# Kernel tuning notes

Hardware: AMD Instinct MI355X
Metric: run time of the kernel (lower is better)

Reference implementation:

```python
import jax, jax.numpy as jnp
import numpy as np
import math

B, TU, TM, D, H = 4, 2048, 256, 1024, 16
DH = D // H
PAIRS = D // 2
LAM = 0.7
EPS_PHASE = 1e-8


def balance_norm(x, w, b, bal_w):
    mu = x.mean(-1, keepdims=True)
    var = ((x - mu) ** 2).mean(-1, keepdims=True)
    normed = (x - mu) / jnp.sqrt(var + 1e-6) * w + b
    half = x.shape[-1] // 2
    e1 = (x[..., :half] ** 2).mean(-1, keepdims=True)
    e2 = (x[..., half:] ** 2).mean(-1, keepdims=True)
    imb = (e1 - e2) * bal_w  # (B,T,1)
    corr = jnp.concatenate([
        jnp.broadcast_to(-imb, x[..., :half].shape),
        jnp.broadcast_to(imb, x[..., half:].shape)], axis=-1)
    return normed + corr


def phase_resonance(a, b):
    # a: (B,Tq,D), b: (B,Tk,D). mean_p cos(th_a - th_b) == (cosA@cosB^T + sinA@sinB^T)/pairs
    def to_phase(x):
        x2 = x.reshape(*x.shape[:-1], PAIRS, 2)
        return jnp.arctan2(x2[..., 1] + EPS_PHASE, x2[..., 0] + EPS_PHASE)
    ta, tb = to_phase(a), to_phase(b)
    ca, sa = jnp.cos(ta), jnp.sin(ta)
    cb, sb = jnp.cos(tb), jnp.sin(tb)
    r = (jnp.einsum('bqp,bkp->bqk', ca, cb) + jnp.einsum('bqp,bkp->bqk', sa, sb)) / PAIRS
    return r


def mha(q_in, kv_in, wq, wk, wv, wo, a_gate, e_gate):
    Bq, Tq, _ = q_in.shape
    Tk = kv_in.shape[1]
    q = (q_in @ wq.T).reshape(Bq, Tq, H, DH)
    k = (kv_in @ wk.T).reshape(Bq, Tk, H, DH)
    v = (kv_in @ wv.T).reshape(Bq, Tk, H, DH)
    scores = jnp.einsum('bqhd,bkhd->bhqk', q, k) / math.sqrt(DH)
    attn = jax.nn.softmax(scores, axis=-1)
    ag = a_gate[:, None, :, :]              # (B,1,Tq,1)
    eg = jnp.swapaxes(e_gate[:, None], 2, 3)  # (B,1,1,Tk)
    attn = attn * ag * eg
    attn = attn / (attn.sum(-1, keepdims=True) + 1e-8)
    ctx = jnp.einsum('bhqk,bkhd->bqhd', attn, v).reshape(Bq, Tq, D)
    return ctx @ wo.T


def setup_inputs() -> dict:
    key = jax.random.key(0)
    ks = jax.random.split(key, 16)
    s = 0.02
    return {
        'o_micro': jax.random.normal(ks[0], (B, TU, D), jnp.float32),
        'o_macro': jax.random.normal(ks[1], (B, TM, D), jnp.float32),
        'r_conv_acc': jax.random.normal(ks[2], (B, TM, TU), jnp.float32) * 0.1,
        'r_emer_acc': jax.random.normal(ks[3], (B, TU, TM), jnp.float32) * 0.1,
        'ln_u_w': jnp.ones((D,), jnp.float32),
        'ln_u_b': jnp.zeros((D,), jnp.float32),
        'bw_u': jnp.float32(0.01),
        'ln_m_w': jnp.ones((D,), jnp.float32),
        'ln_m_b': jnp.zeros((D,), jnp.float32),
        'bw_m': jnp.float32(0.01),
        'gu_w': jax.random.normal(ks[4], (1, D), jnp.float32) * s,
        'gu_b': jnp.zeros((1,), jnp.float32),
        'gm_w': jax.random.normal(ks[5], (1, D), jnp.float32) * s,
        'gm_b': jnp.zeros((1,), jnp.float32),
        'conv_q_w': jax.random.normal(ks[6], (D, D), jnp.float32) * s,
        'conv_k_w': jax.random.normal(ks[7], (D, D), jnp.float32) * s,
        'conv_v_w': jax.random.normal(ks[8], (D, D), jnp.float32) * s,
        'conv_out_w': jax.random.normal(ks[9], (D, D), jnp.float32) * s,
        'emer_q_w': jax.random.normal(ks[10], (D, D), jnp.float32) * s,
        'emer_k_w': jax.random.normal(ks[11], (D, D), jnp.float32) * s,
        'emer_v_w': jax.random.normal(ks[12], (D, D), jnp.float32) * s,
        'emer_out_w': jax.random.normal(ks[13], (D, D), jnp.float32) * s,
        'res_alpha': jnp.float32(1.0),
    }


def reference(o_micro, o_macro, r_conv_acc, r_emer_acc,
              ln_u_w, ln_u_b, bw_u, ln_m_w, ln_m_b, bw_m,
              gu_w, gu_b, gm_w, gm_b,
              conv_q_w, conv_k_w, conv_v_w, conv_out_w,
              emer_q_w, emer_k_w, emer_v_w, emer_out_w, res_alpha):
    ou = balance_norm(o_micro, ln_u_w, ln_u_b, bw_u)
    om = balance_norm(o_macro, ln_m_w, ln_m_b, bw_m)
    g_micro = jax.nn.sigmoid(ou @ gu_w.T + gu_b)  # (B,Tu,1)
    g_macro = jax.nn.sigmoid(om @ gm_w.T + gm_b)  # (B,Tm,1)
    r_conv_inst = phase_resonance(om, ou)  # (B,Tm,Tu)
    r_emer_inst = phase_resonance(ou, om)  # (B,Tu,Tm)
    r_conv_new = LAM * r_conv_acc + (1 - LAM) * r_conv_inst
    r_emer_new = LAM * r_emer_acc + (1 - LAM) * r_emer_inst
    r_conv_scalar = jax.nn.sigmoid(res_alpha * r_conv_new.mean(-1, keepdims=True))
    r_emer_scalar = jax.nn.sigmoid(res_alpha * r_emer_new.mean(-1, keepdims=True))
    delta_macro = mha(om, ou, conv_q_w, conv_k_w, conv_v_w, conv_out_w, g_macro, g_micro)
    o_macro_new = o_macro + delta_macro * r_conv_scalar
    delta_micro = mha(ou, om, emer_q_w, emer_k_w, emer_v_w, emer_out_w, g_micro, g_macro)
    o_micro_new = o_micro + delta_micro * r_emer_scalar
    return (o_micro_new, o_macro_new, r_conv_new, r_emer_new)
```

## Files before the change

kernel.cpp:

```cpp
#include <hip/hip_runtime.h>
#include <math.h>

typedef unsigned short u16;
typedef __attribute__((ext_vector_type(8))) short bf16x8;
typedef __attribute__((ext_vector_type(4))) float f32x4;

__device__ __forceinline__ float sigmoidf_(float x) { return 1.0f / (1.0f + __expf(-x)); }
__device__ __forceinline__ u16 f2bf(float v) {
    union { float f; unsigned u; } x; x.f = v;
    unsigned r = x.u + 0x7fffu + ((x.u >> 16) & 1u);
    return (u16)(r >> 16);
}
__device__ __forceinline__ float bf2f(u16 u) {
    union { unsigned u; float f; } x; x.u = ((unsigned)u) << 16; return x.f;
}

#define GLD(src, dst) __builtin_amdgcn_global_load_lds( \
        (const __attribute__((address_space(1))) void*)(src), \
        (__attribute__((address_space(3))) void*)(dst), 16, 0, 0)
#define GLD4(src, dst) __builtin_amdgcn_global_load_lds( \
        (const __attribute__((address_space(1))) void*)(src), \
        (__attribute__((address_space(3))) void*)(dst), 4, 0, 0)

__global__ void __launch_bounds__(256) norm_gate_kernel(
    const float* __restrict__ X,
    const float* __restrict__ w, const float* __restrict__ bvec,
    const float* __restrict__ bw_p,
    const float* __restrict__ gw, const float* __restrict__ gb_p,
    u16* __restrict__ OUT, u16* __restrict__ PN, float* __restrict__ G)
{
    const int row = blockIdx.x * 4 + (threadIdx.x >> 6);
    const int lane = threadIdx.x & 63;
    const float* xr = X + (size_t)row * 1024 + lane * 16;
    float4 xa = ((const float4*)xr)[0];
    float4 xb = ((const float4*)xr)[1];
    float4 xc = ((const float4*)xr)[2];
    float4 xd = ((const float4*)xr)[3];
    float s1 = (xa.x + xa.y + xa.z + xa.w) + (xb.x + xb.y + xb.z + xb.w)
             + (xc.x + xc.y + xc.z + xc.w) + (xd.x + xd.y + xd.z + xd.w);
    float s2 = xa.x * xa.x + xa.y * xa.y + xa.z * xa.z + xa.w * xa.w
             + xb.x * xb.x + xb.y * xb.y + xb.z * xb.z + xb.w * xb.w
             + xc.x * xc.x + xc.y * xc.y + xc.z * xc.z + xc.w * xc.w
             + xd.x * xd.x + xd.y * xd.y + xd.z * xd.z + xd.w * xd.w;
    #pragma unroll
    for (int o = 1; o <= 32; o <<= 1) s1 += __shfl_xor(s1, o);
    float h2 = s2;
    #pragma unroll
    for (int o = 1; o <= 16; o <<= 1) h2 += __shfl_xor(h2, o);
    const float oth = __shfl_xor(h2, 32);
    const float slo = (lane < 32) ? h2 : oth;
    const float shi = (lane < 32) ? oth : h2;
    const float mu = s1 * (1.0f / 1024.0f);
    const float var = (slo + shi) * (1.0f / 1024.0f) - mu * mu;
    const float rstd = rsqrtf(var + 1e-6f);
    const float imb = (slo - shi) * (1.0f / 512.0f) * (*bw_p);
    const float corr = (lane < 32) ? -imb : imb;
    const int i0 = lane * 16;
    const float4* wp = (const float4*)(w + i0);
    const float4* bp = (const float4*)(bvec + i0);
    const float4* gp = (const float4*)(gw + i0);
    float o16[16];
    float gd = 0.0f;
    #pragma unroll
    for (int q = 0; q < 4; ++q) {
        float4 xv = (q == 0) ? xa : (q == 1) ? xb : (q == 2) ? xc : xd;
        float4 wv = wp[q], bv = bp[q], gv = gp[q];
        float t0 = (xv.x - mu) * rstd * wv.x + bv.x + corr;
        float t1 = (xv.y - mu) * rstd * wv.y + bv.y + corr;
        float t2 = (xv.z - mu) * rstd * wv.z + bv.z + corr;
        float t3 = (xv.w - mu) * rstd * wv.w + bv.w + corr;
        gd += t0 * gv.x + t1 * gv.y + t2 * gv.z + t3 * gv.w;
        o16[4 * q + 0] = t0; o16[4 * q + 1] = t1; o16[4 * q + 2] = t2; o16[4 * q + 3] = t3;
    }
    #pragma unroll
    for (int o = 1; o <= 32; o <<= 1) gd += __shfl_xor(gd, o);
    if (lane == 0) G[row] = sigmoidf_(gd + *gb_p);
    u16 ob[16], pn[16];
    #pragma unroll
    for (int j = 0; j < 16; ++j) ob[j] = f2bf(o16[j]);
    #pragma unroll
    for (int j = 0; j < 8; ++j) {
        float px = o16[2 * j] + 1e-8f, py = o16[2 * j + 1] + 1e-8f;
        float rr = rsqrtf(px * px + py * py);
        pn[2 * j] = f2bf(px * rr); pn[2 * j + 1] = f2bf(py * rr);
    }
    *(uint4*)(OUT + (size_t)row * 1024 + i0) = *(uint4*)ob;
    *(uint4*)(OUT + (size_t)row * 1024 + i0 + 8) = *(uint4*)(ob + 8);
    *(uint4*)(PN + (size_t)row * 1024 + i0) = *(uint4*)pn;
    *(uint4*)(PN + (size_t)row * 1024 + i0 + 8) = *(uint4*)(pn + 8);
}

__global__ void __launch_bounds__(256) wconv_kernel(
    const float* w0, const float* w1, const float* w2, const float* w3,
    const float* w4, const float* w5, const float* w6, const float* w7,
    u16* __restrict__ dst)
{
    const float* s;
    switch (blockIdx.y) {
        case 0: s = w0; break; case 1: s = w1; break;
        case 2: s = w2; break; case 3: s = w3; break;
        case 4: s = w4; break; case 5: s = w5; break;
        case 6: s = w6; break; default: s = w7; break;
    }
    long i = (long)blockIdx.x * 1024 + threadIdx.x * 4;
    float4 v = *(const float4*)(s + i);
    u16 o[4] = { f2bf(v.x), f2bf(v.y), f2bf(v.z), f2bf(v.w) };
    *(uint2*)(dst + (long)blockIdx.y * 1048576 + i) = *(uint2*)o;
}

__global__ void __launch_bounds__(256) attn_flash(
    const u16* __restrict__ Q, const u16* __restrict__ K,
    const u16* __restrict__ VT, const float* __restrict__ AG,
    const float* __restrict__ EG, u16* __restrict__ OC,
    int TQ, int TKV, long vbs)
{
    __shared__ __align__(16) u16 shm[21504];
    float* egf = (float*)(shm + 20480);
    const int t = threadIdx.x;
    const int lane = t & 63, w = t >> 6;
    const int l15 = lane & 15, g = lane >> 4;
    const int qt = blockIdx.x, h = blockIdx.y, b = blockIdx.z;
    const long qrow = (long)b * TQ + qt * 64 + w * 16 + l15;
    const u16* Qp = Q + qrow * 1024 + h * 64 + g * 8;
    const bf16x8 qf0 = *(const bf16x8*)(Qp);
    const bf16x8 qf1 = *(const bf16x8*)(Qp + 32);
    const u16* Kp = K + ((long)b * TKV + w * 16 + l15) * 1024 + h * 64 + g * 8;
    const u16* Vp = VT + (long)b * vbs + (long)(h * 64 + w * 16 + l15) * TKV + g * 8;
    const float* egp = EG + (long)b * TKV + lane;

    auto stage = [&](int kvt, int buf) {
        GLD(Kp + (long)kvt * 1024,      shm + buf * 4096 + (w * 2 + 0) * 512);
        GLD(Kp + (long)kvt * 1024 + 32, shm + buf * 4096 + (w * 2 + 1) * 512);
        GLD(Vp + kvt,      shm + 8192 + buf * 4096 + (w * 2 + 0) * 512);
        GLD(Vp + kvt + 32, shm + 8192 + buf * 4096 + (w * 2 + 1) * 512);
        GLD4(egp + kvt, egf + (buf * 4 + w) * 64);
    };

    const int nT = TKV >> 6;
    f32x4 O[4] = {};
    float mrun = -3.0e38f, lrun = 0.0f, serun = 0.0f;
    stage(0, 0);
    for (int i = 0; i < nT; ++i) {
        const int buf = i & 1;
        if (i + 1 < nT) {
            stage((i + 1) << 6, buf ^ 1);
            asm volatile("s_waitcnt vmcnt(5)" ::: "memory");
        } else {
            asm volatile("s_waitcnt vmcnt(0)" ::: "memory");
        }
        __builtin_amdgcn_sched_barrier(0);
        __builtin_amdgcn_s_barrier();
        const u16* kb = shm + buf * 4096;
        const u16* vb = shm + 8192 + buf * 4096;
        f32x4 sa[4] = {};
        #pragma unroll
        for (int kvf = 0; kvf < 4; ++kvf) {
            bf16x8 kf = *(const bf16x8*)(kb + (kvf * 2 + 0) * 512 + lane * 8);
            sa[kvf] = __builtin_amdgcn_mfma_f32_16x16x32_bf16(kf, qf0, sa[kvf], 0, 0, 0);
        }
        #pragma unroll
        for (int kvf = 0; kvf < 4; ++kvf) {
            bf16x8 kf = *(const bf16x8*)(kb + (kvf * 2 + 1) * 512 + lane * 8);
            sa[kvf] = __builtin_amdgcn_mfma_f32_16x16x32_bf16(kf, qf1, sa[kvf], 0, 0, 0);
        }
        float ev[4][4];
        float tmax = -3.0e38f;
        #pragma unroll
        for (int kvf = 0; kvf < 4; ++kvf)
            #pragma unroll
            for (int j = 0; j < 4; ++j) {
                float s = sa[kvf][j] * 0.125f;
                ev[kvf][j] = s;
                tmax = fmaxf(tmax, s);
            }
        tmax = fmaxf(tmax, __shfl_xor(tmax, 16));
        tmax = fmaxf(tmax, __shfl_xor(tmax, 32));
        const float mnew = fmaxf(mrun, tmax);
        const float corr = __expf(mrun - mnew);
        mrun = mnew;
        float suml = 0.0f, sumg = 0.0f;
        unsigned pk[4][2];
        #pragma unroll
        for (int kvf = 0; kvf < 4; ++kvf) {
            float4 eg4 = *(const float4*)(egf + (buf * 4 + w) * 64 + kvf * 16 + 4 * g);
            float e0 = __expf(ev[kvf][0] - mnew);
            float e1 = __expf(ev[kvf][1] - mnew);
            float e2 = __expf(ev[kvf][2] - mnew);
            float e3 = __expf(ev[kvf][3] - mnew);
            suml += (e0 + e1) + (e2 + e3);
            float g0 = e0 * eg4.x, g1 = e1 * eg4.y, g2 = e2 * eg4.z, g3 = e3 * eg4.w;
            sumg += (g0 + g1) + (g2 + g3);
            pk[kvf][0] = (unsigned)f2bf(g0) | ((unsigned)f2bf(g1) << 16);
            pk[kvf][1] = (unsigned)f2bf(g2) | ((unsigned)f2bf(g3) << 16);
        }
        suml += __shfl_xor(suml, 16); suml += __shfl_xor(suml, 32);
        sumg += __shfl_xor(sumg, 16); sumg += __shfl_xor(sumg, 32);
        lrun = lrun * corr + suml;
        serun = serun * corr + sumg;
        #pragma unroll
        for (int fd = 0; fd < 4; ++fd)
            #pragma unroll
            for (int j = 0; j < 4; ++j) O[fd][j] *= corr;
        u16* pw = shm + 16384 + w * 1024;
        #pragma unroll
        for (int kvf = 0; kvf < 4; ++kvf) {
            const int base = (kvf >> 1) * 512
                           + (l15 + 16 * (2 * (kvf & 1) + (g >> 1))) * 8
                           + 4 * (g & 1);
            *(unsigned*)(pw + base) = pk[kvf][0];
            *(unsigned*)(pw + base + 2) = pk[kvf][1];
        }
        #pragma unroll
        for (int ksv = 0; ksv < 2; ++ksv) {
            bf16x8 pf = *(const bf16x8*)(pw + ksv * 512 + lane * 8);
            #pragma unroll
            for (int fd = 0; fd < 4; ++fd) {
                bf16x8 vf = *(const bf16x8*)(vb + (fd * 2 + ksv) * 512 + lane * 8);
                O[fd] = __builtin_amdgcn_mfma_f32_16x16x32_bf16(vf, pf, O[fd], 0, 0, 0);
            }
        }
        if (i + 1 < nT) __builtin_amdgcn_s_barrier();
    }
    const float agv = AG[qrow];
    const float fac = agv / (agv * serun + lrun * 1e-8f);
    __syncthreads();
    u16* tw = shm + w * 1152;
    #pragma unroll
    for (int fd = 0; fd < 4; ++fd) {
        const int d0 = fd * 16 + 4 * g;
        unsigned v01 = (unsigned)f2bf(O[fd][0] * fac) | ((unsigned)f2bf(O[fd][1] * fac) << 16);
        unsigned v23 = (unsigned)f2bf(O[fd][2] * fac) | ((unsigned)f2bf(O[fd][3] * fac) << 16);
        *(unsigned*)(tw + l15 * 72 + d0) = v01;
        *(unsigned*)(tw + l15 * 72 + d0 + 2) = v23;
    }
    const int qr = lane >> 2, part = lane & 3;
    uint4 va = *(const uint4*)(tw + qr * 72 + part * 16);
    uint4 vb2 = *(const uint4*)(tw + qr * 72 + part * 16 + 8);
    u16* op = OC + ((long)b * TQ + qt * 64 + w * 16 + qr) * 1024 + h * 64 + part * 16;
    *(uint4*)(op) = va;
    *(uint4*)(op + 8) = vb2;
}

#define PHASE(BUF, MQ, NQ, STAGESTMT, VM) do { \
    bf16x8 af_[4][2], bf_[NRC][2]; \
    _Pragma("unroll") for (int fr_ = 0; fr_ < 4; ++fr_) \
      _Pragma("unroll") for (int kk_ = 0; kk_ < 2; ++kk_) \
        af_[fr_][kk_] = *(const bf16x8*)(sh + (BUF) * BUFSZ + (MQ) * 8192 + (wm * 4 + fr_) * 1024 + kk_ * 512 + lane * 8); \
    _Pragma("unroll") for (int fc_ = 0; fc_ < NRC; ++fc_) \
      _Pragma("unroll") for (int kk_ = 0; kk_ < 2; ++kk_) \
        bf_[fc_][kk_] = *(const bf16x8*)(sh + (BUF) * BUFSZ + 16384 + (NQ) * BHALF + (wn * NRC + fc_) * 1024 + kk_ * 512 + lane * 8); \
    STAGESTMT \
    __builtin_amdgcn_s_barrier(); \
    asm volatile("s_waitcnt lgkmcnt(0)" ::: "memory"); \
    __builtin_amdgcn_sched_barrier(0); \
    __builtin_amdgcn_s_setprio(1); \
    _Pragma("unroll") for (int fr_ = 0; fr_ < 4; ++fr_) \
      _Pragma("unroll") for (int fc_ = 0; fc_ < NRC; ++fc_) \
        _Pragma("unroll") for (int kk_ = 0; kk_ < 2; ++kk_) \
          acc[(MQ) * 4 + fr_][(NQ) * NRC + fc_] = __builtin_amdgcn_mfma_f32_16x16x32_bf16( \
              af_[fr_][kk_], bf_[fc_][kk_], acc[(MQ) * 4 + fr_][(NQ) * NRC + fc_], 0, 0, 0); \
    __builtin_amdgcn_s_setprio(0); \
    __builtin_amdgcn_sched_barrier(0); \
    if ((VM) == 1) { \
        if constexpr (BN == 256) asm volatile("s_waitcnt vmcnt(4)" ::: "memory"); \
        else                     asm volatile("s_waitcnt vmcnt(3)" ::: "memory"); \
    } else if ((VM) == 2) { asm volatile("s_waitcnt vmcnt(0)" ::: "memory"); } \
    __builtin_amdgcn_s_barrier(); \
} while (0)

template<int BN, int EPI>
__global__ void __launch_bounds__(512, 1) mfma256(
    const u16* __restrict__ A, const u16* __restrict__ B,
    void* __restrict__ C, void* __restrict__ Cx, void* __restrict__ Cy,
    int K, int lda, int ldb,
    const float* __restrict__ base, const float* __restrict__ rs)
{
    constexpr int NRC = BN / 128;
    constexpr int BHALF = BN * 32;
    constexpr int BUFSZ = 16384 + 2 * BHALF;
    extern __shared__ u16 sh[];
    const int gx = gridDim.x, gy = gridDim.y;
    const int lin = blockIdx.x + gx * blockIdx.y;
    const int xcd = lin & 7, off = lin >> 3;
    const int lby = gy >> 3;
    const int by = xcd * lby + (off % lby);
    const int bx = off / lby;
    const int t = threadIdx.x;
    const int lane = t & 63, w = t >> 6;
    const int wm = w >> 2, wn = w & 3;
    const long m0 = (long)by * 256;
    const long n0 = (long)bx * BN;
    const int l15 = lane & 15, g = lane >> 4;

    auto stageA = [&](int h, int kt, int buf) {
        const long kb = (long)kt * 64 + g * 8;
        #pragma unroll
        for (int r2 = 0; r2 < 2; ++r2) {
            const int c = w + 8 * r2;
            const int sub = c >> 1, kc = c & 1;
            GLD(A + (m0 + h * 128 + sub * 16 + l15) * lda + kb + kc * 32,
                sh + buf * BUFSZ + h * 8192 + c * 512);
        }
    };
    auto stageB = [&](int h, int kt, int buf) {
        const long kb = (long)kt * 64 + g * 8;
        if constexpr (BN == 256) {
            #pragma unroll
            for (int r2 = 0; r2 < 2; ++r2) {
                const int c = w + 8 * r2;
                const int sub = c >> 1, kc = c & 1;
                GLD(B + (n0 + h * 128 + sub * 16 + l15) * ldb + kb + kc * 32,
                    sh + buf * BUFSZ + 16384 + h * BHALF + c * 512);
            }
        } else {
            const int c = w;
            const int sub = c >> 1, kc = c & 1;
            GLD(B + (n0 + h * 64 + sub * 16 + l15) * ldb + kb + kc * 32,
                sh + buf * BUFSZ + 16384 + h * BHALF + c * 512);
        }
    };

    const int nkt = K >> 6, nIter = K >> 7;
    f32x4 acc[8][2 * NRC] = {};

    stageA(0, 0, 0); stageA(1, 0, 0); stageB(0, 0, 0); stageB(1, 0, 0);
    stageA(0, 1, 1); stageA(1, 1, 1); stageB(0, 1, 1); stageB(1, 1, 1);
    if constexpr (BN == 256) asm volatile("s_waitcnt vmcnt(8)" ::: "memory");
    else                     asm volatile("s_waitcnt vmcnt(6)" ::: "memory");
    __builtin_amdgcn_sched_barrier(0);
    __builtin_amdgcn_s_barrier();

    for (int i = 0; i < nIter; ++i) {
        const int kt2 = 2 * i + 2, kt3 = 2 * i + 3;
        const bool s2 = kt2 < nkt, s3 = kt3 < nkt;
        PHASE(0, 0, 0, { if (i > 0) stageA(0, 2 * i + 1, 1); }, 0);
        PHASE(0, 1, 0, { if (i > 0) stageB(1, 2 * i + 1, 1); }, 0);
        PHASE(0, 1, 1, { if (s2) stageB(0, kt2, 0); }, 0);
        PHASE(0, 0, 1, { if (s2) stageA(1, kt2, 0); }, s2 ? 1 : 2);
        PHASE(1, 0, 0, { if (s2) { stageA(0, kt2, 0); stageB(1, kt2, 0); } }, 0);
        PHASE(1, 1, 0, {}, 0);
        PHASE(1, 1, 1, { if (s3) stageB(0, kt3, 1); }, 0);
        PHASE(1, 0, 1, { if (s3) stageA(1, kt3, 1); }, 1);
    }

    #pragma unroll
    for (int mq = 0; mq < 2; ++mq)
    #pragma unroll
    for (int fr = 0; fr < 4; ++fr)
    #pragma unroll
    for (int nq = 0; nq < 2; ++nq)
    #pragma unroll
    for (int fc = 0; fc < NRC; ++fc) {
        const long grow0 = m0 + mq * 128 + wm * 64 + fr * 16 + g * 4;
        const long gcol = n0 + nq * (BN / 2) + wn * (16 * NRC) + fc * 16 + l15;
        const f32x4 a = acc[mq * 4 + fr][nq * NRC + fc];
        if constexpr (EPI == 3) {
            #pragma unroll
            for (int j = 0; j < 4; ++j) {
                const long idx = (grow0 + j) * 1024 + gcol;
                ((float*)C)[idx] = base[idx] + a[j] * rs[grow0 + j];
            }
        } else {
            const int sec = (int)(n0 >> 10);
            if (sec == 0) {
                #pragma unroll
                for (int j = 0; j < 4; ++j)
                    ((u16*)C)[(grow0 + j) * 1024 + gcol] = f2bf(a[j]);
            } else if (sec == 1) {
                const long col = gcol - 1024;
                u16 pk[4] = { f2bf(a[0]), f2bf(a[1]), f2bf(a[2]), f2bf(a[3]) };
                const long idx = (grow0 >> 11) * 2097152 + col * 2048 + (grow0 & 2047);
                *(uint2*)&((u16*)Cx)[idx] = *(uint2*)pk;
            } else {
                #pragma unroll
                for (int j = 0; j < 4; ++j)
                    ((u16*)Cy)[(grow0 + j) * 1024 + (gcol - 2048)] = f2bf(a[j]);
            }
        }
    }
}

template<int BN, int EPI, bool SWZ>
__global__ void __launch_bounds__(256) mfma_nt(
    const u16* __restrict__ A, long zAb, long zAh,
    const u16* __restrict__ B, long zBb, long zBh,
    void* __restrict__ C, long zCb, long zCh,
    void* __restrict__ Cx, void* __restrict__ Cy,
    int K, int lda, int ldb, int ldc, float alpha, int nH, int nsplit,
    const float* __restrict__ base, const float* __restrict__ rs,
    const float* __restrict__ accB, float* __restrict__ OT,
    long zOT, int ldt)
{
    constexpr int NR = BN / 32;
    constexpr int ABUF = 128 * 32;
    constexpr int BBUF = BN * 32;
    __shared__ __align__(16) u16 sh[3 * (ABUF + BBUF)];
    u16* const Ab0 = sh;
    u16* const Bb0 = sh + 3 * ABUF;
    int bx, by, bz;
    if constexpr (SWZ) {
        const int gx = gridDim.x, gy = gridDim.y;
        const int lin = blockIdx.x + gx * blockIdx.y;
        const int xcd = lin & 7, c = lin >> 3;
        const int LBY = gy >> 3;
        const int SPB = 4 * LBY;
        const int sc = c / SPB, rr = c - sc * SPB;
        const int byl = rr >> 2, bxl = rr & 3;
        by = xcd * LBY + byl;
        bx = sc * 4 + bxl;
        bz = 0;
    } else {
        bx = blockIdx.x; by = blockIdx.y; bz = blockIdx.z;
    }
    const int t = threadIdx.x;
    const int lane = t & 63, w = t >> 6;
    const int wr = w >> 1, wc = w & 1;
    const int slab = bz / nsplit, ks = bz - slab * nsplit;
    const int b = slab / nH, h = slab - b * nH;
    const int kchunk = K / nsplit;
    const int kbeg = ks * kchunk, kend = kbeg + kchunk;
    const long m0 = (long)by * 128;
    const long n0 = (long)bx * BN;
    const int frow = lane & 15, fko = (lane >> 4) * 8;
    const u16* gaA = A + zAb * b + zAh * h + (m0 + 32 * w + frow) * lda + fko;
    const u16* gbB;
    if constexpr (BN == 128) gbB = B + zBb * b + zBh * h + (n0 + 32 * w + frow) * ldb + fko;
    else                     gbB = B + zBb * b + zBh * h + (n0 + 16 * w + frow) * ldb + fko;

    auto stage = [&](int kk, int p) {
        u16* ap = Ab0 + p * ABUF;
        u16* bp = Bb0 + p * BBUF;
        GLD(gaA + kk, ap + 2 * w * 512);
        GLD(gaA + 16L * lda + kk, ap + (2 * w + 1) * 512);
        if constexpr (BN == 128) {
            GLD(gbB + kk, bp + 2 * w * 512);
            GLD(gbB + 16L * ldb + kk, bp + (2 * w + 1) * 512);
        } else {
            GLD(gbB + kk, bp + w * 512);
        }
    };

    const int nIter = (kend - kbeg) >> 5;
    f32x4 acc[4][NR] = {};
    stage(kbeg, 0);
    if (nIter > 1) stage(kbeg + 32, 1);
    int cur = 0;
    for (int i = 0; i < nIter; ++i) {
        if (i + 2 < nIter) {
            int p2 = cur + 2; if (p2 >= 3) p2 -= 3;
            stage(kbeg + (i + 2) * 32, p2);
            if constexpr (BN == 128) asm volatile("s_waitcnt vmcnt(8)" ::: "memory");
            else                     asm volatile("s_waitcnt vmcnt(6)" ::: "memory");
        } else if (i + 1 < nIter) {
            if constexpr (BN == 128) asm volatile("s_waitcnt vmcnt(4)" ::: "memory");
            else                     asm volatile("s_waitcnt vmcnt(3)" ::: "memory");
        } else {
            asm volatile("s_waitcnt vmcnt(0)" ::: "memory");
        }
        __builtin_amdgcn_sched_barrier(0);
        __builtin_amdgcn_s_barrier();
        __builtin_amdgcn_sched_barrier(0);
        const u16* ap = Ab0 + cur * ABUF;
        const u16* bp = Bb0 + cur * BBUF;
        bf16x8 af[4], bfr[NR];
        #pragma unroll
        for (int m = 0; m < 4; ++m)
            af[m] = *(const bf16x8*)(ap + (wr * 4 + m) * 512 + lane * 8);
        #pragma unroll
        for (int n = 0; n < NR; ++n)
            bfr[n] = *(const bf16x8*)(bp + (wc * NR + n) * 512 + lane * 8);
        asm volatile("s_waitcnt lgkmcnt(0)" ::: "memory");
        __builtin_amdgcn_sched_barrier(0);
        __builtin_amdgcn_s_barrier();
        #pragma unroll
        for (int m = 0; m < 4; ++m)
            #pragma unroll
            for (int n = 0; n < NR; ++n)
                acc[m][n] = __builtin_amdgcn_mfma_f32_16x16x32_bf16(af[m], bfr[n], acc[m][n], 0, 0, 0);
        cur = (cur == 2) ? 0 : cur + 1;
    }
    const long Coff = zCb * b + zCh * h;
    const int l15 = lane & 15, l4 = lane >> 4;
    #pragma unroll
    for (int m = 0; m < 4; ++m) {
        #pragma unroll
        for (int n = 0; n < NR; ++n) {
            #pragma unroll
            for (int j = 0; j < 4; ++j) {
                const long grow = m0 + wr * 64 + m * 16 + l4 * 4 + j;
                const long gcol = n0 + wc * (BN / 2) + n * 16 + l15;
                const float v = acc[m][n][j] * alpha;
                if constexpr (EPI == 3) {
                    const long idx = grow * ldc + gcol;
                    ((float*)C)[idx] = base[idx] + v * rs[grow];
                } else if constexpr (EPI == 5) {
                    const long idx = Coff + grow * ldc + gcol;
                    ((float*)C)[idx] = 0.7f * base[idx] + 0.3f * v;
                    const long tidx = zOT * b + gcol * (long)ldt + grow;
                    OT[tidx] = 0.7f * accB[tidx] + 0.3f * v;
                } else if constexpr (EPI == 7) {
                    const int sec = (int)(n0 >> 10);
                    if (sec == 0) ((u16*)C)[grow * 1024 + gcol] = f2bf(v);
                    else if (sec == 1) ((u16*)Cx)[grow * 1024 + (gcol - 1024)] = f2bf(v);
                    else {
                        const long col = gcol - 2048;
                        ((u16*)Cy)[(grow >> 8) * 262144 + col * 256 + (grow & 255)] = f2bf(v);
                    }
                }
            }
        }
    }
}

__global__ void __launch_bounds__(256) rowmean_sig_kernel(
    const float* __restrict__ X, int len, float invlen,
    const float* __restrict__ alpha_p, float* __restrict__ OUT)
{
    const int row = blockIdx.x * 4 + (threadIdx.x >> 6);
    const int lane = threadIdx.x & 63;
    const float* xr = X + (long)row * len;
    float s = 0.0f;
    for (int k = lane; k < len; k += 64) s += xr[k];
    for (int o = 32; o > 0; o >>= 1) s += __shfl_xor(s, o);
    if (lane == 0) OUT[row] = sigmoidf_((*alpha_p) * s * invlen);
}

#define MFMA_TAIL nullptr, nullptr, nullptr, nullptr, 0L, 0

extern "C" void kernel_launch(void* const* d_in, const int* in_sizes, int n_in,
                              void* d_out, int out_size, void* d_ws, size_t ws_size,
                              hipStream_t stream)
{
    (void)in_sizes; (void)n_in; (void)out_size; (void)ws_size;
    const float* o_micro    = (const float*)d_in[0];
    const float* o_macro    = (const float*)d_in[1];
    const float* r_conv_acc = (const float*)d_in[2];
    const float* r_emer_acc = (const float*)d_in[3];
    const float* ln_u_w = (const float*)d_in[4];
    const float* ln_u_b = (const float*)d_in[5];
    const float* bw_u   = (const float*)d_in[6];
    const float* ln_m_w = (const float*)d_in[7];
    const float* ln_m_b = (const float*)d_in[8];
    const float* bw_m   = (const float*)d_in[9];
    const float* gu_w   = (const float*)d_in[10];
    const float* gu_b   = (const float*)d_in[11];
    const float* gm_w   = (const float*)d_in[12];
    const float* gm_b   = (const float*)d_in[13];
    const float* wq_c   = (const float*)d_in[14];
    const float* wk_c   = (const float*)d_in[15];
    const float* wv_c   = (const float*)d_in[16];
    const float* wo_c   = (const float*)d_in[17];
    const float* wq_e   = (const float*)d_in[18];
    const float* wk_e   = (const float*)d_in[19];
    const float* wv_e   = (const float*)d_in[20];
    const float* wo_e   = (const float*)d_in[21];
    const float* res_alpha = (const float*)d_in[22];

    float* out = (float*)d_out;
    float* out_micro = out;
    float* out_macro = out + 8388608;
    float* out_rconv = out + 9437184;
    float* out_remer = out + 11534336;

    float* ws = (float*)d_ws;
    u16* OUb = (u16*)ws;
    u16* OMb = (u16*)(ws + 4194304);
    u16* WB  = (u16*)(ws + 4718592);
    u16* Kcb = (u16*)(ws + 8912896);
    u16* VTc = (u16*)(ws + 13107200);
    u16* Qeb = (u16*)(ws + 17301504);
    u16* Qcb = (u16*)(ws + 21495808);
    u16* Keb = (u16*)(ws + 22020096);
    u16* VTe = (u16*)(ws + 22544384);
    u16* PNu = (u16*)(ws + 23068672);
    float* CT = ws + 27262976;
    float* GU = ws + 28311552;
    float* GM = GU + 8192;
    float* RCS = GM + 1024;
    float* RES = RCS + 1024;
    u16* PNm = (u16*)CT;
    u16* CTc = (u16*)CT;
    u16* CTe = Kcb;

    wconv_kernel<<<dim3(1024, 8), 256, 0, stream>>>(wk_c, wv_c, wq_e, wq_c, wk_e, wv_e, wo_c, wo_e, WB);
    norm_gate_kernel<<<2048, 256, 0, stream>>>(o_micro, ln_u_w, ln_u_b, bw_u, gu_w, gu_b, OUb, PNu, GU);
    norm_gate_kernel<<<256, 256, 0, stream>>>(o_macro, ln_m_w, ln_m_b, bw_m, gm_w, gm_b, OMb, PNm, GM);
    mfma_nt<128, 5, false><<<dim3(16, 2, 4), 256, 0, stream>>>(
        PNm, 262144L, 0L, PNu, 2097152L, 0L, out_rconv, 524288L, 0L, nullptr, nullptr,
        1024, 1024, 1024, 2048, 1.0f / 512.0f, 1, 1,
        r_conv_acc, nullptr, r_emer_acc, out_remer, 524288L, 256);
    rowmean_sig_kernel<<<256, 256, 0, stream>>>(out_rconv, 2048, 1.0f / 2048.0f, res_alpha, RCS);
    rowmean_sig_kernel<<<2048, 256, 0, stream>>>(out_remer, 256, 1.0f / 256.0f, res_alpha, RES);
    mfma256<256, 6><<<dim3(12, 32), 512, 131072, stream>>>(
        OUb, WB, Kcb, VTc, Qeb, 1024, 1024, 1024, nullptr, nullptr);
    mfma_nt<128, 7, true><<<dim3(24, 8, 1), 256, 0, stream>>>(
        OMb, 0L, 0L, WB + 3 * 1048576, 0L, 0L, Qcb, 0L, 0L, Keb, VTe,
        1024, 1024, 1024, 1024, 1.0f, 1, 1, MFMA_TAIL);
    attn_flash<<<dim3(4, 16, 4), 256, 0, stream>>>(
        Qcb, Kcb, VTc, GM, GU, CTc, 256, 2048, 2097152L);
    mfma_nt<128, 3, false><<<dim3(8, 8, 1), 256, 0, stream>>>(
        CTc, 0L, 0L, WB + 6 * 1048576, 0L, 0L, out_macro, 0L, 0L, nullptr, nullptr,
        1024, 1024, 1024, 1024, 1.0f, 1, 1, o_macro, RCS, nullptr, nullptr, 0L, 0);
    attn_flash<<<dim3(32, 16, 4), 256, 0, stream>>>(
        Qeb, Keb, VTe, GU, GM, CTe, 2048, 256, 262144L);
    mfma256<128, 3><<<dim3(8, 32), 512, 98304, stream>>>(
        CTe, WB + 7 * 1048576, out_micro, nullptr, nullptr,
        1024, 1024, 1024, o_micro, RES);
}
```

Measured before the change: 303.2 us.

## Reuse A/B register fragments across phases and restage GEMM prefetch schedule

Restructures the 256-row MFMA GEMM main loop so LDS fragments of A and B are loaded once and reused across two consecutive quarter-tile phases (snake order 00,01,11,10) instead of re-reading both per phase. It also reorders the global-to-LDS prefetch so whole k-tiles are staged earlier, and loosens the vmcnt waits to keep more loads in flight. This cuts LDS read traffic and is meant to overlap memory transfers better, at the cost of more live registers and a riskier buffer-reuse ordering.

```diff
diff --git a/kernel.cpp b/kernel.cpp
--- a/kernel.cpp
+++ b/kernel.cpp
@@ -241,29 +241,35 @@
     *(uint4*)(op + 8) = vb2;
 }
 
-#define PHASE(BUF, MQ, NQ, STAGESTMT, VM) do { \
-    bf16x8 af_[4][2], bf_[NRC][2]; \
+#define RD_A(BUF, MQ) do { \
     _Pragma("unroll") for (int fr_ = 0; fr_ < 4; ++fr_) \
-      _Pragma("unroll") for (int kk_ = 0; kk_ < 2; ++kk_) \
-        af_[fr_][kk_] = *(const bf16x8*)(sh + (BUF) * BUFSZ + (MQ) * 8192 + (wm * 4 + fr_) * 1024 + kk_ * 512 + lane * 8); \
+    _Pragma("unroll") for (int kk_ = 0; kk_ < 2; ++kk_) \
+        af[fr_][kk_] = *(const bf16x8*)(sh + (BUF) * BUFSZ + (MQ) * 8192 + (wm * 4 + fr_) * 1024 + kk_ * 512 + lane * 8); \
+} while (0)
+#define RD_B(BUF, NQ, DST) do { \
     _Pragma("unroll") for (int fc_ = 0; fc_ < NRC; ++fc_) \
-      _Pragma("unroll") for (int kk_ = 0; kk_ < 2; ++kk_) \
-        bf_[fc_][kk_] = *(const bf16x8*)(sh + (BUF) * BUFSZ + 16384 + (NQ) * BHALF + (wn * NRC + fc_) * 1024 + kk_ * 512 + lane * 8); \
-    STAGESTMT \
+    _Pragma("unroll") for (int kk_ = 0; kk_ < 2; ++kk_) \
+        DST[fc_][kk_] = *(const bf16x8*)(sh + (BUF) * BUFSZ + 16384 + (NQ) * BHALF + (wn * NRC + fc_) * 1024 + kk_ * 512 + lane * 8); \
+} while (0)
+#define MM(SRC, MQ, NQ) do { \
+    __builtin_amdgcn_s_setprio(1); \
+    _Pragma("unroll") for (int fr_ = 0; fr_ < 4; ++fr_) \
+    _Pragma("unroll") for (int fc_ = 0; fc_ < NRC; ++fc_) \
+    _Pragma("unroll") for (int kk_ = 0; kk_ < 2; ++kk_) \
+        acc[(MQ) * 4 + fr_][(NQ) * NRC + fc_] = __builtin_amdgcn_mfma_f32_16x16x32_bf16( \
+            af[fr_][kk_], SRC[fc_][kk_], acc[(MQ) * 4 + fr_][(NQ) * NRC + fc_], 0, 0, 0); \
+    __builtin_amdgcn_s_setprio(0); \
+} while (0)
+#define FENCE1() do { \
     __builtin_amdgcn_s_barrier(); \
     asm volatile("s_waitcnt lgkmcnt(0)" ::: "memory"); \
     __builtin_amdgcn_sched_barrier(0); \
-    __builtin_amdgcn_s_setprio(1); \
-    _Pragma("unroll") for (int fr_ = 0; fr_ < 4; ++fr_) \
-      _Pragma("unroll") for (int fc_ = 0; fc_ < NRC; ++fc_) \
-        _Pragma("unroll") for (int kk_ = 0; kk_ < 2; ++kk_) \
-          acc[(MQ) * 4 + fr_][(NQ) * NRC + fc_] = __builtin_amdgcn_mfma_f32_16x16x32_bf16( \
-              af_[fr_][kk_], bf_[fc_][kk_], acc[(MQ) * 4 + fr_][(NQ) * NRC + fc_], 0, 0, 0); \
-    __builtin_amdgcn_s_setprio(0); \
+} while (0)
+#define FENCE2(VM) do { \
     __builtin_amdgcn_sched_barrier(0); \
     if ((VM) == 1) { \
-        if constexpr (BN == 256) asm volatile("s_waitcnt vmcnt(4)" ::: "memory"); \
-        else                     asm volatile("s_waitcnt vmcnt(3)" ::: "memory"); \
+        if constexpr (BN == 256) asm volatile("s_waitcnt vmcnt(8)" ::: "memory"); \
+        else                     asm volatile("s_waitcnt vmcnt(6)" ::: "memory"); \
     } else if ((VM) == 2) { asm volatile("s_waitcnt vmcnt(0)" ::: "memory"); } \
     __builtin_amdgcn_s_barrier(); \
 } while (0)
@@ -320,8 +326,9 @@
         }
     };
 
-    const int nkt = K >> 6, nIter = K >> 7;
+    const int nIter = K >> 7;
     f32x4 acc[8][2 * NRC] = {};
+    bf16x8 af[4][2], bf0[NRC][2], bf1[NRC][2];
 
     stageA(0, 0, 0); stageA(1, 0, 0); stageB(0, 0, 0); stageB(1, 0, 0);
     stageA(0, 1, 1); stageA(1, 1, 1); stageB(0, 1, 1); stageB(1, 1, 1);
@@ -331,16 +338,28 @@
     __builtin_amdgcn_s_barrier();
 
     for (int i = 0; i < nIter; ++i) {
-        const int kt2 = 2 * i + 2, kt3 = 2 * i + 3;
-        const bool s2 = kt2 < nkt, s3 = kt3 < nkt;
-        PHASE(0, 0, 0, { if (i > 0) stageA(0, 2 * i + 1, 1); }, 0);
-        PHASE(0, 1, 0, { if (i > 0) stageB(1, 2 * i + 1, 1); }, 0);
-        PHASE(0, 1, 1, { if (s2) stageB(0, kt2, 0); }, 0);
-        PHASE(0, 0, 1, { if (s2) stageA(1, kt2, 0); }, s2 ? 1 : 2);
-        PHASE(1, 0, 0, { if (s2) { stageA(0, kt2, 0); stageB(1, kt2, 0); } }, 0);
-        PHASE(1, 1, 0, {}, 0);
-        PHASE(1, 1, 1, { if (s3) stageB(0, kt3, 1); }, 0);
-        PHASE(1, 0, 1, { if (s3) stageA(1, kt3, 1); }, 1);
+        const bool pre = (i + 1 < nIter);
+        const int ktA = 2 * i + 2, ktB = 2 * i + 3;
+        RD_A(0, 0); RD_B(0, 0, bf0);
+        FENCE1(); MM(bf0, 0, 0); FENCE2(0);
+        RD_B(0, 1, bf1);
+        if (pre) { stageA(0, ktA, 0); stageB(0, ktA, 0); }
+        FENCE1(); MM(bf1, 0, 1); FENCE2(0);
+        RD_A(0, 1);
+        if (pre) stageB(1, ktA, 0);
+        FENCE1(); MM(bf1, 1, 1); FENCE2(0);
+        if (pre) stageA(1, ktA, 0);
+        FENCE1(); MM(bf0, 1, 0); FENCE2(pre ? 1 : 2);
+        RD_A(1, 0); RD_B(1, 0, bf0);
+        FENCE1(); MM(bf0, 0, 0); FENCE2(0);
+        RD_B(1, 1, bf1);
+        if (pre) { stageA(0, ktB, 1); stageB(0, ktB, 1); }
+        FENCE1(); MM(bf1, 0, 1); FENCE2(0);
+        RD_A(1, 1);
+        if (pre) stageB(1, ktB, 1);
+        FENCE1(); MM(bf1, 1, 1); FENCE2(0);
+        if (pre) stageA(1, ktB, 1);
+        FENCE1(); MM(bf0, 1, 0); FENCE2(pre ? 1 : 0);
     }
 
     #pragma unroll
@@ -379,6 +398,11 @@
         }
     }
 }
+#undef RD_A
+#undef RD_B
+#undef MM
+#undef FENCE1
+#undef FENCE2
 
 template<int BN, int EPI, bool SWZ>
 __global__ void __launch_bounds__(256) mfma_nt(
```

Result: no change. 299.2 us (-1.3%).
